# Kernel tuning notes

Hardware: AMD Instinct MI355X
Metric: run time of the kernel (lower is better)

Reference implementation:

```python
import jax, jax.numpy as jnp
import numpy as np

B, S, DQK, DV, H = 4, 2048, 128, 128, 8


def setup_inputs() -> dict:
    key = jax.random.key(0)
    ks = jax.random.split(key, 9)
    s = 0.02
    return {
        "query": jax.random.normal(ks[0], (B, S, DQK), jnp.float32),
        "key": jax.random.normal(ks[1], (B, S, DQK), jnp.float32),
        "value": jax.random.normal(ks[2], (B, S, DV), jnp.float32),
        "WQ": jax.random.normal(ks[3], (DQK, H * DQK), jnp.float32) * s,
        "bQ": jax.random.normal(ks[4], (H * DQK,), jnp.float32) * s,
        "WK": jax.random.normal(ks[5], (DQK, H * DQK), jnp.float32) * s,
        "bK": jax.random.normal(ks[6], (H * DQK,), jnp.float32) * s,
        "WV": jax.random.normal(ks[7], (DV, H * DV), jnp.float32) * s,
        "bV": jax.random.normal(ks[8], (H * DV,), jnp.float32) * s,
    }


def reference(query, key, value, WQ, bQ, WK, bK, WV, bV):
    b, qn, dqk = query.shape
    kn = key.shape[1]
    dv = value.shape[2]
    h = H
    # projections -> [b, n, h, d]
    Q = (query @ WQ + bQ).reshape(b, qn, h, dqk)
    K = (key @ WK + bK).reshape(b, kn, h, dqk)
    V = (value @ WV + bV).reshape(b, kn, h, dv)
    # abs(QK^T)/sqrt(dk) score -- non-standard, prevents flash kernels
    scores = jnp.abs(jnp.einsum("bqhd,bkhd->bhqk", Q, K)) / jnp.sqrt(
        jnp.asarray(dqk, query.dtype)
    )
    w = jax.nn.softmax(scores, axis=-1)  # [b,h,q,k]
    # (complex cast +0j in the original is numerically a no-op on real V)
    out = jnp.einsum("bhqk,bkhd->bqhd", w, V).reshape(b, qn, h * dv)
    return out
```

## Files before the change

kernel.cpp:

```cpp
#include <hip/hip_runtime.h>
#include <hip/hip_bf16.h>

#define B_ 4
#define S_ 2048
#define D_ 128
#define H_ 8

typedef __attribute__((ext_vector_type(8))) short bf16x8;
typedef __attribute__((ext_vector_type(4))) float f32x4;

__device__ __forceinline__ short f2bf(float f) {
  union { float f; unsigned u; } v; v.f = f;
  unsigned u = v.u;
  unsigned r = (u + 0x7FFFu + ((u >> 16) & 1u)) >> 16;
  return (short)r;
}

__device__ __forceinline__ short4 pack4(f32x4 p) {
  union { __hip_bfloat162 h2[2]; short4 s4; } u;
  u.h2[0] = __float22bfloat162_rn(make_float2(p[0], p[1]));
  u.h2[1] = __float22bfloat162_rn(make_float2(p[2], p[3]));
  return u.s4;
}

__device__ __forceinline__ void dma16(const short* g, short* l) {
  __builtin_amdgcn_global_load_lds(
      (const __attribute__((address_space(1))) unsigned int*)g,
      (__attribute__((address_space(3))) unsigned int*)l, 16, 0, 0);
}

__global__ __launch_bounds__(256) void prep(
    const float* __restrict__ WQ, const float* __restrict__ WK, const float* __restrict__ WV,
    short* __restrict__ FQ, short* __restrict__ FK, short* __restrict__ FV) {
  __shared__ float tile[64][65];
  int bw = blockIdx.x >> 5;
  int tl = blockIdx.x & 31;
  int n0 = (tl & 15) * 64, k0 = (tl >> 4) * 64;
  const float* W = (bw == 0) ? WQ : (bw == 1) ? WK : WV;
  short* WF = (bw == 0) ? FQ : (bw == 1) ? FK : FV;
#pragma unroll
  for (int i = 0; i < 16; ++i) {
    int cix = threadIdx.x + 256 * i;
    int rr = cix >> 6, cc = cix & 63;
    tile[rr][cc] = W[(k0 + rr) * 1024 + n0 + cc];
  }
  __syncthreads();
#pragma unroll
  for (int i = 0; i < 16; ++i) {
    int cix = threadIdx.x + 256 * i;
    int rr = cix >> 6, cc = cix & 63;
    int n = n0 + rr, k = k0 + cc;
    size_t off = (size_t)(n >> 7) * 16384
               + (size_t)(((n >> 4) & 7) * 4 + (k >> 5)) * 512
               + ((k >> 3) & 3) * 128 + (n & 15) * 8 + (k & 7);
    WF[off] = f2bf(tile[cc][rr]);
  }
}

template <int MODE>
__device__ __forceinline__ void proj_pair(const float* __restrict__ X,
                                          const short* __restrict__ WF,
                                          const float* __restrict__ bias,
                                          short* __restrict__ out,
                                          int mtile, int np, short* sA) {
  int tid = threadIdx.x;
  int lane = tid & 63, w = tid >> 6;
  int l15 = lane & 15, l4 = lane >> 4;
  int m0 = mtile * 128;

#pragma unroll
  for (int j = 0; j < 8; ++j) {
    int f = w * 8 + j;
    const float* src = X + (size_t)(m0 + (f >> 2) * 16 + l15) * 128 + (f & 3) * 32 + l4 * 8;
    float4 v0 = *(const float4*)src;
    float4 v1 = *(const float4*)(src + 4);
    union { struct { short4 lo, hi; } s; bf16x8 v; } u;
    u.s.lo = pack4((f32x4){v0.x, v0.y, v0.z, v0.w});
    u.s.hi = pack4((f32x4){v1.x, v1.y, v1.z, v1.w});
    *(bf16x8*)(sA + f * 512 + lane * 8) = u.v;
  }

  int wr = w >> 1, wc = w & 1;

  __syncthreads();

  bf16x8 a[4][4];
#pragma unroll
  for (int mi = 0; mi < 4; ++mi)
#pragma unroll
    for (int st = 0; st < 4; ++st)
      a[mi][st] = *(const bf16x8*)(sA + ((wr * 4 + mi) * 4 + st) * 512 + lane * 8);

#pragma unroll
  for (int nt = 0; nt < 2; ++nt) {
    int ntile = np * 2 + nt;
    int n0 = ntile * 128;

    const short* wfb = WF + (size_t)ntile * 16384 + wc * 8192 + lane * 8;
    bf16x8 b[16];
#pragma unroll
    for (int q = 0; q < 16; ++q)
      b[q] = *(const bf16x8*)(wfb + q * 512);

    f32x4 acc[4][4];
#pragma unroll
    for (int mi = 0; mi < 4; ++mi)
#pragma unroll
      for (int ni = 0; ni < 4; ++ni) acc[mi][ni] = (f32x4){0.f, 0.f, 0.f, 0.f};

#pragma unroll
    for (int mi = 0; mi < 4; ++mi) {
#pragma unroll
      for (int ni = 0; ni < 4; ++ni) {
#pragma unroll
        for (int st = 0; st < 4; ++st) {
          if (MODE <= 1)
            acc[mi][ni] = __builtin_amdgcn_mfma_f32_16x16x32_bf16(b[ni * 4 + st], a[mi][st], acc[mi][ni], 0, 0, 0);
          else
            acc[mi][ni] = __builtin_amdgcn_mfma_f32_16x16x32_bf16(a[mi][st], b[ni * 4 + st], acc[mi][ni], 0, 0, 0);
        }
      }
    }

    if (MODE == 0) {
#pragma unroll
      for (int mi = 0; mi < 4; ++mi) {
        int sg = m0 + wr * 64 + mi * 16 + l15;
        int bb = sg >> 11, s = sg & 2047;
        short* orow = out + ((size_t)(bb * H_ + ntile) * S_ + s) * D_;
#pragma unroll
        for (int ni = 0; ni < 4; ++ni) {
          int d0 = wc * 64 + ni * 16 + l4 * 4;
          float4 bv = *(const float4*)(bias + n0 + d0);
          f32x4 t = acc[mi][ni];
          t[0] += bv.x; t[1] += bv.y; t[2] += bv.z; t[3] += bv.w;
          *(short4*)(orow + d0) = pack4(t);
        }
      }
    } else if (MODE == 1) {
#pragma unroll
      for (int mi = 0; mi < 4; ++mi) {
        int key = m0 + wr * 64 + mi * 16 + l15;
        int bb = key >> 11, kk = key & 2047;
        size_t base = (size_t)(bb * H_ + ntile) * (S_ * D_) + (size_t)(kk >> 6) * 8192
                    + ((kk >> 4) & 3) * 2048 + (kk & 15) * 8;
#pragma unroll
        for (int ni = 0; ni < 4; ++ni) {
          int d0 = wc * 64 + ni * 16 + l4 * 4;
          float4 bv = *(const float4*)(bias + n0 + d0);
          f32x4 t = acc[mi][ni];
          t[0] += bv.x; t[1] += bv.y; t[2] += bv.z; t[3] += bv.w;
          size_t off = base + (size_t)(d0 >> 5) * 512 + ((d0 >> 3) & 3) * 128 + (d0 & 7);
          *(short4*)(out + off) = pack4(t);
        }
      }
    } else {
#pragma unroll
      for (int ni = 0; ni < 4; ++ni) {
        int d = wc * 64 + ni * 16 + l15;
        float bvs = bias[n0 + d];
#pragma unroll
        for (int mi = 0; mi < 4; ++mi) {
          int sg0 = m0 + wr * 64 + mi * 16 + l4 * 4;
          int bb = sg0 >> 11, s0 = sg0 & 2047;
          f32x4 t = acc[mi][ni];
          t[0] += bvs; t[1] += bvs; t[2] += bvs; t[3] += bvs;
          size_t off = (size_t)(bb * H_ + ntile) * (S_ * D_)
                     + (size_t)(s0 >> 6) * 8192
                     + (size_t)((d >> 4) * 2 + ((s0 >> 5) & 1)) * 512
                     + ((s0 >> 3) & 3) * 128 + (d & 15) * 8
                     + (s0 & 7);
          *(short4*)(out + off) = pack4(t);
        }
      }
    }
  }
}

__global__ __launch_bounds__(256, 3) void proj3(
    const float* __restrict__ xq, const float* __restrict__ xk, const float* __restrict__ xv,
    const short* __restrict__ wtq, const short* __restrict__ wtk, const short* __restrict__ wtv,
    const float* __restrict__ bQ, const float* __restrict__ bK, const float* __restrict__ bV,
    short* __restrict__ Qp, short* __restrict__ Kf, short* __restrict__ Vf) {
  __shared__ short sA[16384];
  int work = (blockIdx.x & 7) * 96 + (blockIdx.x >> 3);
  int which = work >> 8;
  int t = work & 255;
  int mtile = t >> 2, np = t & 3;
  if (which == 0)      proj_pair<0>(xq, wtq, bQ, Qp, mtile, np, sA);
  else if (which == 1) proj_pair<1>(xk, wtk, bK, Kf, mtile, np, sA);
  else                 proj_pair<2>(xv, wtv, bV, Vf, mtile, np, sA);
}

#define PSTR 72

#define QK_H(KR)                                                               \
  _Pragma("unroll") for (int m = 0; m < 2; ++m) {                              \
    s0[m] = (f32x4){0.f, 0.f, 0.f, 0.f};                                       \
    s1[m] = (f32x4){0.f, 0.f, 0.f, 0.f};                                       \
    _Pragma("unroll") for (int st = 0; st < 4; ++st) {                         \
      s0[m] = __builtin_amdgcn_mfma_f32_16x16x32_bf16(KR[m * 4 + st], aq[0][st], s0[m], 0, 0, 0); \
      s1[m] = __builtin_amdgcn_mfma_f32_16x16x32_bf16(KR[m * 4 + st], aq[1][st], s1[m], 0, 0, 0); \
    }                                                                          \
  }

#define SM_H()                                                                 \
  _Pragma("unroll") for (int m = 0; m < 2; ++m) {                              \
    _Pragma("unroll") for (int r = 0; r < 4; ++r) {                            \
      float p = __builtin_amdgcn_exp2f(fabsf(s0[m][r]) * SC2);                 \
      ls0 += p;                                                                \
      s0[m][r] = p;                                                            \
    }                                                                          \
    *(short4*)(pw0 + l15 * PSTR + m * 16 + l4 * 4) = pack4(s0[m]);             \
  }                                                                            \
  _Pragma("unroll") for (int m = 0; m < 2; ++m) {                              \
    _Pragma("unroll") for (int r = 0; r < 4; ++r) {                            \
      float p = __builtin_amdgcn_exp2f(fabsf(s1[m][r]) * SC2);                 \
      ls1 += p;                                                                \
      s1[m][r] = p;                                                            \
    }                                                                          \
    *(short4*)(pw1 + l15 * PSTR + m * 16 + l4 * 4) = pack4(s1[m]);             \
  }                                                                            \
  ap0 = *(const bf16x8*)(pw0 + l15 * PSTR + l4 * 8);                           \
  ap1 = *(const bf16x8*)(pw1 + l15 * PSTR + l4 * 8);

#define PV_H()                                                                 \
  _Pragma("unroll") for (int t8 = 0; t8 < 8; ++t8) {                           \
    o0[t8] = __builtin_amdgcn_mfma_f32_16x16x32_bf16(ap0, bv[t8], o0[t8], 0, 0, 0); \
    o1[t8] = __builtin_amdgcn_mfma_f32_16x16x32_bf16(ap1, bv[t8], o1[t8], 0, 0, 0); \
  }

__global__ __launch_bounds__(512, 2) void attn(const short* __restrict__ Qp,
                                               const short* __restrict__ Kf,
                                               const short* __restrict__ Vf,
                                               float* __restrict__ out) {
  __shared__ short sK0[8192], sK1[8192];
  __shared__ short sV0[8192], sV1[8192];
  __shared__ short sP[16 * 16 * PSTR];

  int tid = threadIdx.x;
  int lane = tid & 63, w = tid >> 6;
  int xcd = blockIdx.x & 7;
  int idx = blockIdx.x >> 3;
  int bh  = xcd * 4 + (idx & 3);
  int qt  = idx >> 2;
  int q0  = qt * 256;
  int l15 = lane & 15, l4 = lane >> 4;

  const short* Qbase = Qp + (size_t)bh * S_ * D_;
  const short* kgs = Kf + (size_t)bh * S_ * D_ + 2 * w * 512 + lane * 8;
  const short* vgs = Vf + (size_t)bh * S_ * D_ + 2 * w * 512 + lane * 8;

  dma16(kgs,       sK0 + 2 * w * 512);
  dma16(kgs + 512, sK0 + (2 * w + 1) * 512);
  dma16(vgs,       sV0 + 2 * w * 512);
  dma16(vgs + 512, sV0 + (2 * w + 1) * 512);

  bf16x8 aq[2][4];
#pragma unroll
  for (int g = 0; g < 2; ++g)
#pragma unroll
    for (int st = 0; st < 4; ++st)
      aq[g][st] = *(const bf16x8*)(Qbase + (q0 + w * 32 + g * 16 + l15) * D_ + l4 * 8 + 32 * st);

  f32x4 o0[8], o1[8];
#pragma unroll
  for (int t = 0; t < 8; ++t) {
    o0[t] = (f32x4){0.f, 0.f, 0.f, 0.f};
    o1[t] = (f32x4){0.f, 0.f, 0.f, 0.f};
  }
  float ls0 = 0.f, ls1 = 0.f;

  const float SC2 = 0.127530637f;
  short* pw0 = sP + w * 16 * PSTR;
  short* pw1 = sP + (8 + w) * 16 * PSTR;

  __syncthreads();

  for (int t = 0; t < 32; ++t) {
    const short* sKc = (t & 1) ? sK1 : sK0;
    const short* sVc = (t & 1) ? sV1 : sV0;
    if (t < 31) {
      short* sKn = (t & 1) ? sK0 : sK1;
      short* sVn = (t & 1) ? sV0 : sV1;
      const short* kn = kgs + (size_t)(t + 1) * 8192;
      const short* vn = vgs + (size_t)(t + 1) * 8192;
      dma16(kn,       sKn + 2 * w * 512);
      dma16(kn + 512, sKn + (2 * w + 1) * 512);
      dma16(vn,       sVn + 2 * w * 512);
      dma16(vn + 512, sVn + (2 * w + 1) * 512);
    }
    bf16x8 kA[8], kB[8], bv[8];
#pragma unroll
    for (int j = 0; j < 8; ++j)
      kA[j] = *(const bf16x8*)(sKc + j * 512 + lane * 8);
#pragma unroll
    for (int j = 0; j < 8; ++j)
      kB[j] = *(const bf16x8*)(sKc + 4096 + j * 512 + lane * 8);
#pragma unroll
    for (int j = 0; j < 8; ++j)
      bv[j] = *(const bf16x8*)(sVc + (2 * j) * 512 + lane * 8);
    __builtin_amdgcn_sched_barrier(0);

    f32x4 s0[2], s1[2];
    bf16x8 ap0, ap1;
    __builtin_amdgcn_s_setprio(1);
    QK_H(kA);
    __builtin_amdgcn_s_setprio(0);
    SM_H();
    __builtin_amdgcn_s_setprio(1);
    PV_H();
    __builtin_amdgcn_s_setprio(0);
#pragma unroll
    for (int j = 0; j < 8; ++j)
      bv[j] = *(const bf16x8*)(sVc + (2 * j + 1) * 512 + lane * 8);
    __builtin_amdgcn_s_setprio(1);
    QK_H(kB);
    __builtin_amdgcn_s_setprio(0);
    SM_H();
    __builtin_amdgcn_s_setprio(1);
    PV_H();
    __builtin_amdgcn_s_setprio(0);
    __syncthreads();
  }

  ls0 += __shfl_xor(ls0, 16);
  ls0 += __shfl_xor(ls0, 32);
  ls1 += __shfl_xor(ls1, 16);
  ls1 += __shfl_xor(ls1, 32);
  float inv0[4], inv1[4];
#pragma unroll
  for (int r = 0; r < 4; ++r) {
    inv0[r] = 1.f / __shfl(ls0, l4 * 4 + r);
    inv1[r] = 1.f / __shfl(ls1, l4 * 4 + r);
  }

  int bb = bh >> 3, h = bh & 7;
#pragma unroll
  for (int t = 0; t < 8; ++t) {
#pragma unroll
    for (int r = 0; r < 4; ++r) {
      int qA = q0 + w * 32 + l4 * 4 + r;
      int qB = qA + 16;
      out[((size_t)(bb * S_ + qA)) * (H_ * D_) + h * D_ + t * 16 + l15] = o0[t][r] * inv0[r];
      out[((size_t)(bb * S_ + qB)) * (H_ * D_) + h * D_ + t * 16 + l15] = o1[t][r] * inv1[r];
    }
  }
}

extern "C" void kernel_launch(void* const* d_in, const int* in_sizes, int n_in,
                              void* d_out, int out_size, void* d_ws, size_t ws_size,
                              hipStream_t stream) {
  (void)in_sizes; (void)n_in; (void)out_size; (void)ws_size;
  const float* q  = (const float*)d_in[0];
  const float* k  = (const float*)d_in[1];
  const float* v  = (const float*)d_in[2];
  const float* WQ = (const float*)d_in[3];
  const float* bQ = (const float*)d_in[4];
  const float* WK = (const float*)d_in[5];
  const float* bK = (const float*)d_in[6];
  const float* WV = (const float*)d_in[7];
  const float* bV = (const float*)d_in[8];

  const int NW = D_ * H_ * D_;
  const int NP = B_ * H_ * S_ * D_;

  short* ws  = (short*)d_ws;
  short* wtq = ws;
  short* wtk = wtq + NW;
  short* wtv = wtk + NW;
  short* Qp  = wtv + NW;
  short* Kf  = Qp + NP;
  short* Vf  = Kf + NP;

  prep<<<96, 256, 0, stream>>>(WQ, WK, WV, wtq, wtk, wtv);

  proj3<<<768, 256, 0, stream>>>(q, k, v, wtq, wtk, wtv, bQ, bK, bV, Qp, Kf, Vf);

  attn<<<256, 512, 0, stream>>>(Qp, Kf, Vf, (float*)d_out);
}
```

Before: 184.9 us.

## Stage projection outputs through LDS for coalesced 16-byte global stores

```diff
diff --git a/kernel.cpp b/kernel.cpp
--- a/kernel.cpp
+++ b/kernel.cpp
@@ -67,6 +67,8 @@
   int lane = tid & 63, w = tid >> 6;
   int l15 = lane & 15, l4 = lane >> 4;
   int m0 = mtile * 128;
+  int bb = m0 >> 11;
+  int mloc = m0 & 2047;
 
 #pragma unroll
   for (int j = 0; j < 8; ++j) {
@@ -97,10 +99,6 @@
     int n0 = ntile * 128;
 
     const short* wfb = WF + (size_t)ntile * 16384 + wc * 8192 + lane * 8;
-    bf16x8 b[16];
-#pragma unroll
-    for (int q = 0; q < 16; ++q)
-      b[q] = *(const bf16x8*)(wfb + q * 512);
 
     f32x4 acc[4][4];
 #pragma unroll
@@ -109,49 +107,50 @@
       for (int ni = 0; ni < 4; ++ni) acc[mi][ni] = (f32x4){0.f, 0.f, 0.f, 0.f};
 
 #pragma unroll
-    for (int mi = 0; mi < 4; ++mi) {
-#pragma unroll
-      for (int ni = 0; ni < 4; ++ni) {
+    for (int ni = 0; ni < 4; ++ni) {
+      bf16x8 bfr[4];
+#pragma unroll
+      for (int st = 0; st < 4; ++st)
+        bfr[st] = *(const bf16x8*)(wfb + (ni * 4 + st) * 512);
+#pragma unroll
+      for (int mi = 0; mi < 4; ++mi) {
 #pragma unroll
         for (int st = 0; st < 4; ++st) {
           if (MODE <= 1)
-            acc[mi][ni] = __builtin_amdgcn_mfma_f32_16x16x32_bf16(b[ni * 4 + st], a[mi][st], acc[mi][ni], 0, 0, 0);
+            acc[mi][ni] = __builtin_amdgcn_mfma_f32_16x16x32_bf16(bfr[st], a[mi][st], acc[mi][ni], 0, 0, 0);
           else
-            acc[mi][ni] = __builtin_amdgcn_mfma_f32_16x16x32_bf16(a[mi][st], b[ni * 4 + st], acc[mi][ni], 0, 0, 0);
+            acc[mi][ni] = __builtin_amdgcn_mfma_f32_16x16x32_bf16(a[mi][st], bfr[st], acc[mi][ni], 0, 0, 0);
         }
       }
     }
 
+    __syncthreads();
+
     if (MODE == 0) {
 #pragma unroll
       for (int mi = 0; mi < 4; ++mi) {
-        int sg = m0 + wr * 64 + mi * 16 + l15;
-        int bb = sg >> 11, s = sg & 2047;
-        short* orow = out + ((size_t)(bb * H_ + ntile) * S_ + s) * D_;
+        int lrow = wr * 64 + mi * 16 + l15;
 #pragma unroll
         for (int ni = 0; ni < 4; ++ni) {
           int d0 = wc * 64 + ni * 16 + l4 * 4;
           float4 bv = *(const float4*)(bias + n0 + d0);
           f32x4 t = acc[mi][ni];
           t[0] += bv.x; t[1] += bv.y; t[2] += bv.z; t[3] += bv.w;
-          *(short4*)(orow + d0) = pack4(t);
+          *(short4*)(sA + lrow * 128 + d0) = pack4(t);
         }
       }
     } else if (MODE == 1) {
 #pragma unroll
       for (int mi = 0; mi < 4; ++mi) {
-        int key = m0 + wr * 64 + mi * 16 + l15;
-        int bb = key >> 11, kk = key & 2047;
-        size_t base = (size_t)(bb * H_ + ntile) * (S_ * D_) + (size_t)(kk >> 6) * 8192
-                    + ((kk >> 4) & 3) * 2048 + (kk & 15) * 8;
+        int lk = wr * 64 + mi * 16 + l15;
+        int kbase = (lk >> 6) * 8192 + ((lk >> 4) & 3) * 2048 + (lk & 15) * 8;
 #pragma unroll
         for (int ni = 0; ni < 4; ++ni) {
           int d0 = wc * 64 + ni * 16 + l4 * 4;
           float4 bv = *(const float4*)(bias + n0 + d0);
           f32x4 t = acc[mi][ni];
           t[0] += bv.x; t[1] += bv.y; t[2] += bv.z; t[3] += bv.w;
-          size_t off = base + (size_t)(d0 >> 5) * 512 + ((d0 >> 3) & 3) * 128 + (d0 & 7);
-          *(short4*)(out + off) = pack4(t);
+          *(short4*)(sA + kbase + (d0 >> 5) * 512 + ((d0 >> 3) & 3) * 128 + (d0 & 7)) = pack4(t);
         }
       }
     } else {
@@ -161,18 +160,27 @@
         float bvs = bias[n0 + d];
 #pragma unroll
         for (int mi = 0; mi < 4; ++mi) {
-          int sg0 = m0 + wr * 64 + mi * 16 + l4 * 4;
-          int bb = sg0 >> 11, s0 = sg0 & 2047;
+          int ls0 = wr * 64 + mi * 16 + l4 * 4;
           f32x4 t = acc[mi][ni];
           t[0] += bvs; t[1] += bvs; t[2] += bvs; t[3] += bvs;
-          size_t off = (size_t)(bb * H_ + ntile) * (S_ * D_)
-                     + (size_t)(s0 >> 6) * 8192
-                     + (size_t)((d >> 4) * 2 + ((s0 >> 5) & 1)) * 512
-                     + ((s0 >> 3) & 3) * 128 + (d & 15) * 8
-                     + (s0 & 7);
-          *(short4*)(out + off) = pack4(t);
+          *(short4*)(sA + (ls0 >> 6) * 8192
+                        + ((d >> 4) * 2 + ((ls0 >> 5) & 1)) * 512
+                        + ((ls0 >> 3) & 3) * 128 + (d & 15) * 8
+                        + (ls0 & 7)) = pack4(t);
         }
       }
+    }
+    __syncthreads();
+
+    short* gdst;
+    if (MODE == 0)
+      gdst = out + ((size_t)(bb * H_ + ntile) * S_ + mloc) * D_;
+    else
+      gdst = out + (size_t)(bb * H_ + ntile) * (S_ * D_) + (size_t)(mloc >> 6) * 8192;
+#pragma unroll
+    for (int i = 0; i < 8; ++i) {
+      bf16x8 vv = *(const bf16x8*)(sA + (i * 256 + tid) * 8);
+      *(bf16x8*)(gdst + (i * 256 + tid) * 8) = vv;
     }
   }
 }
```

Result: faster. 176.2 us, median of 2 (-4.7%).
